# Optimization experiments

Hardware: AMD Instinct MI355X
Metric: run time of the kernel (lower is better)

The kernel has to match this reference:

```python
import jax, jax.numpy as jnp
import numpy as np

EPS = 1e-5  # torch LayerNorm default

def ln(x, g, b):
    mu = jnp.mean(x, axis=-1, keepdims=True)
    var = jnp.mean((x - mu) ** 2, axis=-1, keepdims=True)
    return (x - mu) * jax.lax.rsqrt(var + EPS) * g + b

B, S, E, A = 131072, 199, 3, 32
D_IN = S + 1  # state_dim + 1 (time feature)

def setup_inputs() -> dict:
    key = jax.random.key(0)
    ks = iter(jax.random.split(key, 32))
    def w(shape, fan_in):
        lim = 1.0 / np.sqrt(fan_in)
        return jax.random.uniform(next(ks), shape, jnp.float32, -lim, lim)
    inp = {
        "state": jax.random.normal(next(ks), (B, S), jnp.float32),
        "time_delta": jax.random.uniform(next(ks), (B,), jnp.float32),
        # trunk: Linear(200,256)+LN, Linear(256,256)+LN, Linear(256,128)+LN
        "W1": w((D_IN, 256), D_IN), "b1": w((256,), D_IN),
        "g1": jnp.ones((256,), jnp.float32), "be1": jnp.zeros((256,), jnp.float32),
        "W2": w((256, 256), 256), "b2": w((256,), 256),
        "g2": jnp.ones((256,), jnp.float32), "be2": jnp.zeros((256,), jnp.float32),
        "W3": w((256, 128), 256), "b3": w((128,), 256),
        "g3": jnp.ones((128,), jnp.float32), "be3": jnp.zeros((128,), jnp.float32),
        # value stream
        "Wv1": w((128, 64), 128), "bv1": w((64,), 128),
        "gv": jnp.ones((64,), jnp.float32), "bev": jnp.zeros((64,), jnp.float32),
        "Wv2": w((64, 1), 64), "bv2": w((1,), 64),
        # E stacked advantage streams (all heads share action dim A)
        "Wa1": w((E, 128, 64), 128), "ba1": w((E, 64), 128),
        "ga": jnp.ones((E, 64), jnp.float32), "bea": jnp.zeros((E, 64), jnp.float32),
        "Wa2": w((E, 64, A), 64), "ba2": w((E, A), 64),
        "event_type": jax.random.randint(next(ks), (B,), 0, E),
    }
    return inp

def reference(state, time_delta,
              W1, b1, g1, be1, W2, b2, g2, be2, W3, b3, g3, be3,
              Wv1, bv1, gv, bev, Wv2, bv2,
              Wa1, ba1, ga, bea, Wa2, ba2, event_type):
    td = time_delta[:, None]                       # [B,1]
    x = jnp.concatenate([state, td], axis=1)       # [B,200]
    h = jax.nn.relu(ln(x @ W1 + b1, g1, be1))      # [B,256]
    h = jax.nn.relu(ln(h @ W2 + b2, g2, be2))      # [B,256]
    f = jax.nn.relu(ln(h @ W3 + b3, g3, be3))      # [B,128]
    v = jax.nn.relu(ln(f @ Wv1 + bv1, gv, bev)) @ Wv2 + bv2  # [B,1]
    # compute all E advantage heads, then per-sample select by event_type
    h1 = jnp.einsum('bd,edh->ebh', f, Wa1) + ba1[:, None, :]           # [E,B,64]
    h1 = jax.nn.relu(ln(h1, ga[:, None, :], bea[:, None, :]))
    adv_all = jnp.einsum('ebh,eha->eba', h1, Wa2) + ba2[:, None, :]    # [E,B,A]
    adv = jnp.take_along_axis(adv_all, event_type[None, :, None], axis=0)[0]  # [B,A]
    return v + (adv - adv.mean(axis=1, keepdims=True))
```

## Files before the change

kernel.cpp:

```cpp
#include <hip/hip_runtime.h>
#include <hip/hip_bf16.h>
#include <stdint.h>

#define DEV __device__ __forceinline__

typedef __attribute__((ext_vector_type(8))) short short8;
typedef __attribute__((ext_vector_type(4))) float floatx4;

constexpr int TM  = 64;
constexpr int NB  = 131072;
constexpr int AST = 264;

struct F4 { float x,y,z,w; };

constexpr int OFF_W1 = 0;
constexpr int OFF_W2 = 57344;
constexpr int OFF_W3 = 122880;
constexpr int OFF_WH = 155648;
constexpr int OFF_WA2= 188416;
constexpr int NWQ    = 194560;

constexpr int C_B1=0, C_G1=256, C_BE1=512, C_B2=768, C_G2=1024, C_BE2=1280,
  C_B3=1536, C_G3=1664, C_BE3=1792, C_BV1=1920, C_GV=1984, C_BEV=2048,
  C_WV2=2112, C_BV2=2176, C_BA1=2180, C_GA=2372, C_BEA=2564, C_BA2=2756;
constexpr int NCONST=2852;

struct Ptrs {
  const float *state,*td,*W1,*b1,*g1,*be1,*W2,*b2,*g2,*be2,*W3,*b3,*g3,*be3,
    *Wv1,*bv1,*gv,*bev,*Wv2,*bv2,*Wa1,*ba1,*ga,*bea,*Wa2,*ba2;
  const int *et;
};

DEV unsigned short f2bf(float x){
  uint32_t u = __float_as_uint(x);
  u += 0x7fffu + ((u>>16)&1u);
  return (unsigned short)(u>>16);
}
DEV uint32_t pkbf(float a, float b){
  float2 f2; f2.x=a; f2.y=b;
  __hip_bfloat162 h = __float22bfloat162_rn(f2);
  union { __hip_bfloat162 h; uint32_t u; } cv; cv.h = h;
  return cv.u;
}

__global__ void prep_kernel(Ptrs p, unsigned short* __restrict__ wq, float* __restrict__ cq){
  int idx = blockIdx.x*256 + threadIdx.x;
  if (idx < NWQ) {
    float v = 0.f;
    if (idx < OFF_W2) {
      int e = idx, w = e/14336, r = e%14336;
      int kc = r>>11, ct=(r>>9)&3, l=(r>>3)&63, j=r&7;
      int n = w*64 + ct*16 + (l&15);
      int k = kc*32 + (l>>4)*8 + j;
      if (k < 200) v = p.W1[k*256 + n];
      else if (k == 200) v = p.b1[n];
    } else if (idx < OFF_W3) {
      int e = idx-OFF_W2, w=e>>14, r=e&16383;
      int kc=r>>11, ct=(r>>9)&3, l=(r>>3)&63, j=r&7;
      int n = w*64 + ct*16 + (l&15);
      int k = kc*32 + (l>>4)*8 + j;
      v = p.W2[k*256 + n];
    } else if (idx < OFF_WH) {
      int e = idx-OFF_W3, w=e>>13, r=e&8191;
      int kc=r>>10, ct=(r>>9)&1, l=(r>>3)&63, j=r&7;
      int n = w*32 + ct*16 + (l&15);
      int k = kc*32 + (l>>4)*8 + j;
      v = p.W3[k*128 + n];
    } else if (idx < OFF_WA2) {
      int e = idx-OFF_WH, h=e>>13, r=e&8191;
      int kc=r>>11, ct=(r>>9)&3, l=(r>>3)&63, j=r&7;
      int n = ct*16 + (l&15);
      int k = kc*32 + (l>>4)*8 + j;
      v = (h<3) ? p.Wa1[h*8192 + k*64 + n] : p.Wv1[k*64 + n];
    } else {
      int e = idx-OFF_WA2, h=e>>11, r=e&2047;
      int kc=r>>10, ct=(r>>9)&1, l=(r>>3)&63, j=r&7;
      int n = ct*16 + (l&15);
      int k = kc*32 + (l>>4)*8 + j;
      v = p.Wa2[h*2048 + k*32 + n];
    }
    wq[idx] = f2bf(v);
  } else if (idx < NWQ + NCONST) {
    int ci = idx - NWQ;
    float v;
    if      (ci < 256)  v = p.b1[ci];
    else if (ci < 512)  v = p.g1[ci-256];
    else if (ci < 768)  v = p.be1[ci-512];
    else if (ci < 1024) v = p.b2[ci-768];
    else if (ci < 1280) v = p.g2[ci-1024];
    else if (ci < 1536) v = p.be2[ci-1280];
    else if (ci < 1664) v = p.b3[ci-1536];
    else if (ci < 1792) v = p.g3[ci-1664];
    else if (ci < 1920) v = p.be3[ci-1792];
    else if (ci < 1984) v = p.bv1[ci-1920];
    else if (ci < 2048) v = p.gv[ci-1984];
    else if (ci < 2112) v = p.bev[ci-2048];
    else if (ci < 2176) v = p.Wv2[ci-2112];
    else if (ci < 2180) v = (ci==2176) ? p.bv2[0] : 0.f;
    else if (ci < 2372) v = p.ba1[ci-2180];
    else if (ci < 2564) v = p.ga[ci-2372];
    else if (ci < 2756) v = p.bea[ci-2564];
    else                v = p.ba2[ci-2756];
    cq[ci] = v;
  }
}

template<int RT>
DEV void zeroAccT(floatx4 (&acc)[RT][4]){
  const floatx4 z = {0.f,0.f,0.f,0.f};
  #pragma unroll
  for (int rt=0;rt<RT;rt++)
    #pragma unroll
    for (int ct=0;ct<4;ct++) acc[rt][ct]=z;
}

template<int KC,int RT>
DEV void runGemmW(floatx4 (&acc)[RT][4], const unsigned short* __restrict__ wp,
                  const unsigned short* __restrict__ aB, int aOff, int lane){
  #pragma unroll
  for (int kc=0;kc<KC;kc++){
    short8 a[4];
    #pragma unroll
    for (int c=0;c<4;c++)
      a[c] = *(const short8*)(aB + c*16*AST + aOff + kc*32);
    #pragma unroll
    for (int rt=0;rt<RT;rt++){
      short8 bw = *(const short8*)(wp + (kc*RT+rt)*512 + lane*8);
      #pragma unroll
      for (int c=0;c<4;c++)
        acc[rt][c] = __builtin_amdgcn_mfma_f32_16x16x32_bf16(bw, a[c], acc[rt][c], 0,0,0);
    }
  }
}

DEV void gemmL1G(floatx4 (&acc)[4][4], const unsigned short* __restrict__ wp,
                 const float* __restrict__ xb, const float* __restrict__ tdp,
                 int lane){
  const int q=lane>>4, ln=lane&15;
  #pragma unroll
  for (int kc=0;kc<7;kc++){
    short8 bfr[4];
    #pragma unroll
    for (int ct=0;ct<4;ct++){
      const float* rp = xb + (size_t)(ct*16+ln)*199;
      uint32_t w0,w1,w2,w3;
      if (kc<6){
        F4 lo = *(const F4*)(rp + kc*32 + q*8);
        F4 hi = *(const F4*)(rp + kc*32 + q*8 + 4);
        w0=pkbf(lo.x,lo.y); w1=pkbf(lo.z,lo.w); w2=pkbf(hi.x,hi.y); w3=pkbf(hi.z,hi.w);
      } else if (q==0){
        F4 lo = *(const F4*)(rp + 192);
        float v4=rp[196], v5=rp[197], v6=rp[198], v7=tdp[ct*16+ln];
        w0=pkbf(lo.x,lo.y); w1=pkbf(lo.z,lo.w); w2=pkbf(v4,v5); w3=pkbf(v6,v7);
      } else if (q==1){
        w0=0x3F80u; w1=0u; w2=0u; w3=0u;
      } else {
        w0=0u; w1=0u; w2=0u; w3=0u;
      }
      union { uint32_t u[4]; short8 s; } cv;
      cv.u[0]=w0; cv.u[1]=w1; cv.u[2]=w2; cv.u[3]=w3;
      bfr[ct]=cv.s;
    }
    #pragma unroll
    for (int rt=0;rt<4;rt++){
      short8 bw = *(const short8*)(wp + (kc*4+rt)*512 + lane*8);
      #pragma unroll
      for (int c=0;c<4;c++)
        acc[rt][c] = __builtin_amdgcn_mfma_f32_16x16x32_bf16(bw, bfr[c], acc[rt][c], 0,0,0);
    }
  }
}

template<int RT,bool BIAS>
DEV void statsT(floatx4 (&acc)[RT][4], const float* __restrict__ cq, int bo,
                float* sbuf, float* ssbuf, int q, int ln){
  if constexpr (BIAS){
    #pragma unroll
    for (int rt=0;rt<RT;rt++){
      floatx4 b4 = *(const floatx4*)(cq + bo + rt*16 + q*4);
      #pragma unroll
      for (int ct=0;ct<4;ct++) acc[rt][ct] += b4;
    }
  }
  #pragma unroll
  for (int ct=0;ct<4;ct++){
    float s=0.f, ss=0.f;
    #pragma unroll
    for (int rt=0;rt<RT;rt++)
      #pragma unroll
      for (int r=0;r<4;r++){ float v=acc[rt][ct][r]; s+=v; ss+=v*v; }
    s += __shfl_xor(s,16); ss += __shfl_xor(ss,16);
    s += __shfl_xor(s,32); ss += __shfl_xor(ss,32);
    if (q==0){
      atomicAdd(&sbuf[ct*16+ln], s);
      atomicAdd(&ssbuf[ct*16+ln], ss);
    }
  }
}

template<int RT>
DEV void lnWriteT(const floatx4 (&acc)[RT][4], const float* __restrict__ cq, int go, int beo,
                  const float* sbuf, const float* ssbuf, float invN,
                  unsigned short* act_, int colBase, int q, int ln){
  float mu[4], rs[4];
  #pragma unroll
  for (int ct=0;ct<4;ct++){
    float sv = sbuf[ct*16+ln], ssv = ssbuf[ct*16+ln];
    mu[ct] = sv*invN;
    rs[ct] = rsqrtf(ssv*invN - mu[ct]*mu[ct] + 1e-5f);
  }
  #pragma unroll
  for (int rt=0;rt<RT;rt++){
    floatx4 g4  = *(const floatx4*)(cq + go  + rt*16 + q*4);
    floatx4 be4 = *(const floatx4*)(cq + beo + rt*16 + q*4);
    #pragma unroll
    for (int ct=0;ct<4;ct++){
      float y[4];
      #pragma unroll
      for (int r=0;r<4;r++)
        y[r] = fmaxf((acc[rt][ct][r]-mu[ct])*rs[ct]*g4[r]+be4[r], 0.f);
      uint2 pk; pk.x = pkbf(y[0],y[1]); pk.y = pkbf(y[2],y[3]);
      *(uint2*)(act_ + (ct*16+ln)*AST + colBase + rt*16 + q*4) = pk;
    }
  }
}

DEV void headPhase(floatx4 (&acc)[4][4], const float* __restrict__ cq,
                   const unsigned short* __restrict__ wq,
                   const unsigned short* __restrict__ actb, float* vb,
                   int w, int lane, int q, int ln){
  zeroAccT<4>(acc);
  runGemmW<4,4>(acc, wq + OFF_WH + w*8192, actb + ln*AST + q*8, 0, lane);
  const int bo = (w<3)? C_BA1+w*64 : C_BV1;
  const int go = (w<3)? C_GA +w*64 : C_GV;
  const int beo= (w<3)? C_BEA+w*64 : C_BEV;
  #pragma unroll
  for (int rt=0;rt<4;rt++){
    floatx4 b4 = *(const floatx4*)(cq + bo + rt*16 + q*4);
    #pragma unroll
    for (int ct=0;ct<4;ct++) acc[rt][ct] += b4;
  }
  float mu[4], rs[4];
  #pragma unroll
  for (int ct=0;ct<4;ct++){
    float s=0.f, ss=0.f;
    #pragma unroll
    for (int rt=0;rt<4;rt++)
      #pragma unroll
      for (int r=0;r<4;r++){ float v=acc[rt][ct][r]; s+=v; ss+=v*v; }
    s += __shfl_xor(s,16); ss += __shfl_xor(ss,16);
    s += __shfl_xor(s,32); ss += __shfl_xor(ss,32);
    mu[ct]=s*(1.f/64.f);
    rs[ct]=rsqrtf(ss*(1.f/64.f)-mu[ct]*mu[ct]+1e-5f);
  }
  #pragma unroll
  for (int rt=0;rt<4;rt++){
    floatx4 g4  = *(const floatx4*)(cq + go  + rt*16 + q*4);
    floatx4 be4 = *(const floatx4*)(cq + beo + rt*16 + q*4);
    #pragma unroll
    for (int ct=0;ct<4;ct++)
      #pragma unroll
      for (int r=0;r<4;r++)
        acc[rt][ct][r] = fmaxf((acc[rt][ct][r]-mu[ct])*rs[ct]*g4[r]+be4[r], 0.f);
  }
  if (w==3){
    float bv2v = cq[C_BV2];
    floatx4 wv4[4];
    #pragma unroll
    for (int rt=0;rt<4;rt++) wv4[rt] = *(const floatx4*)(cq + C_WV2 + rt*16 + q*4);
    #pragma unroll
    for (int ct=0;ct<4;ct++){
      float dot=0.f;
      #pragma unroll
      for (int rt=0;rt<4;rt++)
        #pragma unroll
        for (int r=0;r<4;r++) dot += acc[rt][ct][r]*wv4[rt][r];
      dot += __shfl_xor(dot,16);
      dot += __shfl_xor(dot,32);
      if (q==0) vb[ct*16+ln] = dot + bv2v;
    }
  }
}

DEV void advPhase(const floatx4 (&acc)[4][4], const float* __restrict__ cq,
                  const unsigned short* __restrict__ wq,
                  unsigned short* actb, const float* vb, const int* etlT,
                  float* __restrict__ outT, int w, int lane, int q, int ln){
  #pragma unroll
  for (int rt=0;rt<4;rt++)
    #pragma unroll
    for (int ct=0;ct<4;ct++){
      uint2 pk;
      pk.x = pkbf(acc[rt][ct][0], acc[rt][ct][1]);
      pk.y = pkbf(acc[rt][ct][2], acc[rt][ct][3]);
      *(uint2*)(actb + (ct*16+ln)*AST + 64*w + rt*16 + q*4) = pk;
    }
  floatx4 acc2[2][4];
  zeroAccT<2>(acc2);
  runGemmW<2,2>(acc2, wq + OFF_WA2 + w*2048, actb + ln*AST + q*8, 64*w, lane);
  #pragma unroll
  for (int rt=0;rt<2;rt++){
    floatx4 b4 = *(const floatx4*)(cq + C_BA2 + w*32 + rt*16 + q*4);
    #pragma unroll
    for (int ct=0;ct<4;ct++) acc2[rt][ct] += b4;
  }
  #pragma unroll
  for (int ct=0;ct<4;ct++){
    float sm=0.f;
    #pragma unroll
    for (int rt=0;rt<2;rt++)
      #pragma unroll
      for (int r=0;r<4;r++) sm += acc2[rt][ct][r];
    sm += __shfl_xor(sm,16);
    sm += __shfl_xor(sm,32);
    int b = ct*16+ln;
    if (etlT[b]==w){
      float vm = vb[b] - sm*(1.f/32.f);
      #pragma unroll
      for (int rt=0;rt<2;rt++){
        floatx4 o = acc2[rt][ct];
        o[0]+=vm; o[1]+=vm; o[2]+=vm; o[3]+=vm;
        *(floatx4*)(outT + (size_t)b*32 + rt*16 + q*4) = o;
      }
    }
  }
}

__global__ __launch_bounds__(256,2) void dqn_main(
    const float* __restrict__ state, const float* __restrict__ td,
    const int* __restrict__ et, const unsigned short* __restrict__ wq,
    const float* __restrict__ cq, float* __restrict__ out)
{
  __shared__ __align__(16) unsigned short actA[TM*AST];
  __shared__ __align__(16) unsigned short actB[TM*AST];
  __shared__ float sstat[2][3][2][64];
  __shared__ float vbuf[2][64];
  __shared__ int   etl[2][64];

  const int tid=threadIdx.x, w=tid>>6, lane=tid&63, q=lane>>4, ln=lane&15;
  const int rowBlk = blockIdx.x*128;
  const float* x0 = state + (size_t)rowBlk*199;
  const float* x1 = x0 + (size_t)64*199;

  ((float*)sstat)[tid]     = 0.f;
  ((float*)sstat)[tid+256] = 0.f;
  ((float*)sstat)[tid+512] = 0.f;
  if (tid < 128) ((int*)etl)[tid] = et[rowBlk+tid];
  __syncthreads();

  floatx4 aT0[4][4], aT1[4][4];

  zeroAccT<4>(aT0);
  gemmL1G(aT0, wq + OFF_W1 + w*14336, x0, td + rowBlk, lane);
  statsT<4,false>(aT0, cq, 0, sstat[0][0][0], sstat[0][0][1], q, ln);
  __syncthreads();

  lnWriteT<4>(aT0, cq, C_G1+w*64, C_BE1+w*64, sstat[0][0][0], sstat[0][0][1], 1.f/256.f, actA, w*64, q, ln);
  zeroAccT<4>(aT1);
  gemmL1G(aT1, wq + OFF_W1 + w*14336, x1, td + rowBlk + 64, lane);
  statsT<4,false>(aT1, cq, 0, sstat[1][0][0], sstat[1][0][1], q, ln);
  __syncthreads();

  lnWriteT<4>(aT1, cq, C_G1+w*64, C_BE1+w*64, sstat[1][0][0], sstat[1][0][1], 1.f/256.f, actB, w*64, q, ln);
  zeroAccT<4>(aT0);
  runGemmW<8,4>(aT0, wq + OFF_W2 + w*16384, actA + ln*AST + q*8, 0, lane);
  statsT<4,true>(aT0, cq, C_B2+w*64, sstat[0][1][0], sstat[0][1][1], q, ln);
  __syncthreads();

  lnWriteT<4>(aT0, cq, C_G2+w*64, C_BE2+w*64, sstat[0][1][0], sstat[0][1][1], 1.f/256.f, actA, w*64, q, ln);
  zeroAccT<4>(aT1);
  runGemmW<8,4>(aT1, wq + OFF_W2 + w*16384, actB + ln*AST + q*8, 0, lane);
  statsT<4,true>(aT1, cq, C_B2+w*64, sstat[1][1][0], sstat[1][1][1], q, ln);
  __syncthreads();

  lnWriteT<4>(aT1, cq, C_G2+w*64, C_BE2+w*64, sstat[1][1][0], sstat[1][1][1], 1.f/256.f, actB, w*64, q, ln);
  floatx4 c3T0[2][4];
  zeroAccT<2>(c3T0);
  runGemmW<8,2>(c3T0, wq + OFF_W3 + w*8192, actA + ln*AST + q*8, 0, lane);
  statsT<2,true>(c3T0, cq, C_B3+w*32, sstat[0][2][0], sstat[0][2][1], q, ln);
  __syncthreads();

  lnWriteT<2>(c3T0, cq, C_G3+w*32, C_BE3+w*32, sstat[0][2][0], sstat[0][2][1], 1.f/128.f, actA, w*32, q, ln);
  floatx4 c3T1[2][4];
  zeroAccT<2>(c3T1);
  runGemmW<8,2>(c3T1, wq + OFF_W3 + w*8192, actB + ln*AST + q*8, 0, lane);
  statsT<2,true>(c3T1, cq, C_B3+w*32, sstat[1][2][0], sstat[1][2][1], q, ln);
  __syncthreads();

  lnWriteT<2>(c3T1, cq, C_G3+w*32, C_BE3+w*32, sstat[1][2][0], sstat[1][2][1], 1.f/128.f, actB, w*32, q, ln);
  headPhase(aT0, cq, wq, actA, vbuf[0], w, lane, q, ln);
  __syncthreads();

  headPhase(aT1, cq, wq, actB, vbuf[1], w, lane, q, ln);
  if (w<3) advPhase(aT0, cq, wq, actA, vbuf[0], etl[0], out + (size_t)rowBlk*32, w, lane, q, ln);
  __syncthreads();

  if (w<3) advPhase(aT1, cq, wq, actB, vbuf[1], etl[1], out + (size_t)(rowBlk+64)*32, w, lane, q, ln);
}

extern "C" void kernel_launch(void* const* d_in, const int* in_sizes, int n_in,
                              void* d_out, int out_size, void* d_ws, size_t ws_size,
                              hipStream_t stream)
{
  Ptrs p;
  p.state=(const float*)d_in[0];  p.td =(const float*)d_in[1];
  p.W1 =(const float*)d_in[2];  p.b1 =(const float*)d_in[3];  p.g1 =(const float*)d_in[4];  p.be1=(const float*)d_in[5];
  p.W2 =(const float*)d_in[6];  p.b2 =(const float*)d_in[7];  p.g2 =(const float*)d_in[8];  p.be2=(const float*)d_in[9];
  p.W3 =(const float*)d_in[10]; p.b3 =(const float*)d_in[11]; p.g3 =(const float*)d_in[12]; p.be3=(const float*)d_in[13];
  p.Wv1=(const float*)d_in[14]; p.bv1=(const float*)d_in[15]; p.gv =(const float*)d_in[16]; p.bev=(const float*)d_in[17];
  p.Wv2=(const float*)d_in[18]; p.bv2=(const float*)d_in[19];
  p.Wa1=(const float*)d_in[20]; p.ba1=(const float*)d_in[21]; p.ga =(const float*)d_in[22]; p.bea=(const float*)d_in[23];
  p.Wa2=(const float*)d_in[24]; p.ba2=(const float*)d_in[25];
  p.et =(const int*)d_in[26];

  unsigned short* wq = (unsigned short*)d_ws;
  float* cq = (float*)((char*)d_ws + (size_t)NWQ*2);

  const int prepN = NWQ + NCONST;
  hipLaunchKernelGGL(prep_kernel, dim3((prepN+255)/256), dim3(256), 0, stream, p, wq, cq);
  hipLaunchKernelGGL(dqn_main, dim3(NB/128), dim3(256), 0, stream,
                     p.state, p.td, p.et, (const unsigned short*)wq, (const float*)cq, (float*)d_out);
}
```

Measured before the change: 291.5 us.

## Process one 64-row tile per block with register weight prefetch and higher occupancy

```diff
diff --git a/kernel.cpp b/kernel.cpp
--- a/kernel.cpp
+++ b/kernel.cpp
@@ -115,6 +115,41 @@
 }
 
 template<int KC,int RT>
+DEV void runGemmPF(floatx4 (&acc)[RT][4], const unsigned short* __restrict__ wp,
+                   const unsigned short* __restrict__ aB, int aOff, int lane,
+                   const short8 (&pf)[4]){
+  constexpr int PFK = 4/RT;
+  constexpr int NBLK = KC/PFK;
+  short8 wcur[4];
+  #pragma unroll
+  for (int i=0;i<4;i++) wcur[i]=pf[i];
+  #pragma unroll
+  for (int blk=0; blk<NBLK; blk++){
+    short8 wnxt[4];
+    if (blk+1 < NBLK){
+      #pragma unroll
+      for (int i=0;i<4;i++)
+        wnxt[i] = *(const short8*)(wp + ((blk+1)*4 + i)*512 + lane*8);
+    }
+    #pragma unroll
+    for (int kk=0;kk<PFK;kk++){
+      const int kc = blk*PFK+kk;
+      short8 a[4];
+      #pragma unroll
+      for (int c=0;c<4;c++)
+        a[c] = *(const short8*)(aB + c*16*AST + aOff + kc*32);
+      #pragma unroll
+      for (int rt=0;rt<RT;rt++)
+        #pragma unroll
+        for (int c=0;c<4;c++)
+          acc[rt][c] = __builtin_amdgcn_mfma_f32_16x16x32_bf16(wcur[kk*RT+rt], a[c], acc[rt][c], 0,0,0);
+    }
+    #pragma unroll
+    for (int i=0;i<4;i++) wcur[i]=wnxt[i];
+  }
+}
+
+template<int KC,int RT>
 DEV void runGemmW(floatx4 (&acc)[RT][4], const unsigned short* __restrict__ wp,
                   const unsigned short* __restrict__ aB, int aOff, int lane){
   #pragma unroll
@@ -133,12 +168,21 @@
   }
 }
 
-DEV void gemmL1G(floatx4 (&acc)[4][4], const unsigned short* __restrict__ wp,
-                 const float* __restrict__ xb, const float* __restrict__ tdp,
-                 int lane){
+DEV void gemmL1Gpf(floatx4 (&acc)[4][4], const unsigned short* __restrict__ wp,
+                   const float* __restrict__ xb, const float* __restrict__ tdp,
+                   int lane, const short8 (&pf)[4]){
   const int q=lane>>4, ln=lane&15;
+  short8 wcur[4];
+  #pragma unroll
+  for (int i=0;i<4;i++) wcur[i]=pf[i];
   #pragma unroll
   for (int kc=0;kc<7;kc++){
+    short8 wnxt[4];
+    if (kc<6){
+      #pragma unroll
+      for (int rt=0;rt<4;rt++)
+        wnxt[rt] = *(const short8*)(wp + ((kc+1)*4+rt)*512 + lane*8);
+    }
     short8 bfr[4];
     #pragma unroll
     for (int ct=0;ct<4;ct++){
@@ -162,18 +206,18 @@
       bfr[ct]=cv.s;
     }
     #pragma unroll
-    for (int rt=0;rt<4;rt++){
-      short8 bw = *(const short8*)(wp + (kc*4+rt)*512 + lane*8);
+    for (int rt=0;rt<4;rt++)
       #pragma unroll
       for (int c=0;c<4;c++)
-        acc[rt][c] = __builtin_amdgcn_mfma_f32_16x16x32_bf16(bw, bfr[c], acc[rt][c], 0,0,0);
-    }
+        acc[rt][c] = __builtin_amdgcn_mfma_f32_16x16x32_bf16(wcur[rt], bfr[c], acc[rt][c], 0,0,0);
+    #pragma unroll
+    for (int i=0;i<4;i++) wcur[i]=wnxt[i];
   }
 }
 
 template<int RT,bool BIAS>
-DEV void statsT(floatx4 (&acc)[RT][4], const float* __restrict__ cq, int bo,
-                float* sbuf, float* ssbuf, int q, int ln){
+DEV void statsS(floatx4 (&acc)[RT][4], const float* __restrict__ cq, int bo,
+                float (*sst)[64][4], int w, int q, int ln){
   if constexpr (BIAS){
     #pragma unroll
     for (int rt=0;rt<RT;rt++){
@@ -192,22 +236,26 @@
     s += __shfl_xor(s,16); ss += __shfl_xor(ss,16);
     s += __shfl_xor(s,32); ss += __shfl_xor(ss,32);
     if (q==0){
-      atomicAdd(&sbuf[ct*16+ln], s);
-      atomicAdd(&ssbuf[ct*16+ln], ss);
+      sst[0][ct*16+ln][w] = s;
+      sst[1][ct*16+ln][w] = ss;
     }
   }
 }
 
 template<int RT>
-DEV void lnWriteT(const floatx4 (&acc)[RT][4], const float* __restrict__ cq, int go, int beo,
-                  const float* sbuf, const float* ssbuf, float invN,
+DEV void lnWriteS(const floatx4 (&acc)[RT][4], const float* __restrict__ cq, int go, int beo,
+                  const float (*sst)[64][4], float invN,
                   unsigned short* act_, int colBase, int q, int ln){
   float mu[4], rs[4];
   #pragma unroll
   for (int ct=0;ct<4;ct++){
-    float sv = sbuf[ct*16+ln], ssv = ssbuf[ct*16+ln];
+    int row = ct*16+ln;
+    floatx4 s4 = *(const floatx4*)&sst[0][row][0];
+    floatx4 q4 = *(const floatx4*)&sst[1][row][0];
+    float sv = s4[0]+s4[1]+s4[2]+s4[3];
+    float qv = q4[0]+q4[1]+q4[2]+q4[3];
     mu[ct] = sv*invN;
-    rs[ct] = rsqrtf(ssv*invN - mu[ct]*mu[ct] + 1e-5f);
+    rs[ct] = rsqrtf(qv*invN - mu[ct]*mu[ct] + 1e-5f);
   }
   #pragma unroll
   for (int rt=0;rt<RT;rt++){
@@ -225,177 +273,159 @@
   }
 }
 
-DEV void headPhase(floatx4 (&acc)[4][4], const float* __restrict__ cq,
-                   const unsigned short* __restrict__ wq,
-                   const unsigned short* __restrict__ actb, float* vb,
-                   int w, int lane, int q, int ln){
-  zeroAccT<4>(acc);
-  runGemmW<4,4>(acc, wq + OFF_WH + w*8192, actb + ln*AST + q*8, 0, lane);
-  const int bo = (w<3)? C_BA1+w*64 : C_BV1;
-  const int go = (w<3)? C_GA +w*64 : C_GV;
-  const int beo= (w<3)? C_BEA+w*64 : C_BEV;
-  #pragma unroll
-  for (int rt=0;rt<4;rt++){
-    floatx4 b4 = *(const floatx4*)(cq + bo + rt*16 + q*4);
-    #pragma unroll
-    for (int ct=0;ct<4;ct++) acc[rt][ct] += b4;
-  }
-  float mu[4], rs[4];
-  #pragma unroll
-  for (int ct=0;ct<4;ct++){
-    float s=0.f, ss=0.f;
-    #pragma unroll
-    for (int rt=0;rt<4;rt++)
-      #pragma unroll
-      for (int r=0;r<4;r++){ float v=acc[rt][ct][r]; s+=v; ss+=v*v; }
-    s += __shfl_xor(s,16); ss += __shfl_xor(ss,16);
-    s += __shfl_xor(s,32); ss += __shfl_xor(ss,32);
-    mu[ct]=s*(1.f/64.f);
-    rs[ct]=rsqrtf(ss*(1.f/64.f)-mu[ct]*mu[ct]+1e-5f);
-  }
-  #pragma unroll
-  for (int rt=0;rt<4;rt++){
-    floatx4 g4  = *(const floatx4*)(cq + go  + rt*16 + q*4);
-    floatx4 be4 = *(const floatx4*)(cq + beo + rt*16 + q*4);
-    #pragma unroll
-    for (int ct=0;ct<4;ct++)
-      #pragma unroll
-      for (int r=0;r<4;r++)
-        acc[rt][ct][r] = fmaxf((acc[rt][ct][r]-mu[ct])*rs[ct]*g4[r]+be4[r], 0.f);
-  }
-  if (w==3){
-    float bv2v = cq[C_BV2];
-    floatx4 wv4[4];
-    #pragma unroll
-    for (int rt=0;rt<4;rt++) wv4[rt] = *(const floatx4*)(cq + C_WV2 + rt*16 + q*4);
-    #pragma unroll
-    for (int ct=0;ct<4;ct++){
-      float dot=0.f;
-      #pragma unroll
-      for (int rt=0;rt<4;rt++)
-        #pragma unroll
-        for (int r=0;r<4;r++) dot += acc[rt][ct][r]*wv4[rt][r];
-      dot += __shfl_xor(dot,16);
-      dot += __shfl_xor(dot,32);
-      if (q==0) vb[ct*16+ln] = dot + bv2v;
-    }
-  }
-}
-
-DEV void advPhase(const floatx4 (&acc)[4][4], const float* __restrict__ cq,
-                  const unsigned short* __restrict__ wq,
-                  unsigned short* actb, const float* vb, const int* etlT,
-                  float* __restrict__ outT, int w, int lane, int q, int ln){
-  #pragma unroll
-  for (int rt=0;rt<4;rt++)
-    #pragma unroll
-    for (int ct=0;ct<4;ct++){
-      uint2 pk;
-      pk.x = pkbf(acc[rt][ct][0], acc[rt][ct][1]);
-      pk.y = pkbf(acc[rt][ct][2], acc[rt][ct][3]);
-      *(uint2*)(actb + (ct*16+ln)*AST + 64*w + rt*16 + q*4) = pk;
-    }
-  floatx4 acc2[2][4];
-  zeroAccT<2>(acc2);
-  runGemmW<2,2>(acc2, wq + OFF_WA2 + w*2048, actb + ln*AST + q*8, 64*w, lane);
-  #pragma unroll
-  for (int rt=0;rt<2;rt++){
-    floatx4 b4 = *(const floatx4*)(cq + C_BA2 + w*32 + rt*16 + q*4);
-    #pragma unroll
-    for (int ct=0;ct<4;ct++) acc2[rt][ct] += b4;
-  }
-  #pragma unroll
-  for (int ct=0;ct<4;ct++){
-    float sm=0.f;
-    #pragma unroll
-    for (int rt=0;rt<2;rt++)
-      #pragma unroll
-      for (int r=0;r<4;r++) sm += acc2[rt][ct][r];
-    sm += __shfl_xor(sm,16);
-    sm += __shfl_xor(sm,32);
-    int b = ct*16+ln;
-    if (etlT[b]==w){
-      float vm = vb[b] - sm*(1.f/32.f);
-      #pragma unroll
-      for (int rt=0;rt<2;rt++){
-        floatx4 o = acc2[rt][ct];
-        o[0]+=vm; o[1]+=vm; o[2]+=vm; o[3]+=vm;
-        *(floatx4*)(outT + (size_t)b*32 + rt*16 + q*4) = o;
-      }
-    }
-  }
-}
-
-__global__ __launch_bounds__(256,2) void dqn_main(
+__global__ __launch_bounds__(256,4) void dqn_main(
     const float* __restrict__ state, const float* __restrict__ td,
     const int* __restrict__ et, const unsigned short* __restrict__ wq,
     const float* __restrict__ cq, float* __restrict__ out)
 {
-  __shared__ __align__(16) unsigned short actA[TM*AST];
-  __shared__ __align__(16) unsigned short actB[TM*AST];
-  __shared__ float sstat[2][3][2][64];
-  __shared__ float vbuf[2][64];
-  __shared__ int   etl[2][64];
+  __shared__ __align__(16) unsigned short act[TM*AST];
+  __shared__ __align__(16) float sstat[2][64][4];
+  __shared__ float vbuf[64];
 
   const int tid=threadIdx.x, w=tid>>6, lane=tid&63, q=lane>>4, ln=lane&15;
-  const int rowBlk = blockIdx.x*128;
+  const int rowBlk = blockIdx.x*TM;
   const float* x0 = state + (size_t)rowBlk*199;
-  const float* x1 = x0 + (size_t)64*199;
-
-  ((float*)sstat)[tid]     = 0.f;
-  ((float*)sstat)[tid+256] = 0.f;
-  ((float*)sstat)[tid+512] = 0.f;
-  if (tid < 128) ((int*)etl)[tid] = et[rowBlk+tid];
-  __syncthreads();
-
-  floatx4 aT0[4][4], aT1[4][4];
-
-  zeroAccT<4>(aT0);
-  gemmL1G(aT0, wq + OFF_W1 + w*14336, x0, td + rowBlk, lane);
-  statsT<4,false>(aT0, cq, 0, sstat[0][0][0], sstat[0][0][1], q, ln);
-  __syncthreads();
-
-  lnWriteT<4>(aT0, cq, C_G1+w*64, C_BE1+w*64, sstat[0][0][0], sstat[0][0][1], 1.f/256.f, actA, w*64, q, ln);
-  zeroAccT<4>(aT1);
-  gemmL1G(aT1, wq + OFF_W1 + w*14336, x1, td + rowBlk + 64, lane);
-  statsT<4,false>(aT1, cq, 0, sstat[1][0][0], sstat[1][0][1], q, ln);
-  __syncthreads();
-
-  lnWriteT<4>(aT1, cq, C_G1+w*64, C_BE1+w*64, sstat[1][0][0], sstat[1][0][1], 1.f/256.f, actB, w*64, q, ln);
-  zeroAccT<4>(aT0);
-  runGemmW<8,4>(aT0, wq + OFF_W2 + w*16384, actA + ln*AST + q*8, 0, lane);
-  statsT<4,true>(aT0, cq, C_B2+w*64, sstat[0][1][0], sstat[0][1][1], q, ln);
-  __syncthreads();
-
-  lnWriteT<4>(aT0, cq, C_G2+w*64, C_BE2+w*64, sstat[0][1][0], sstat[0][1][1], 1.f/256.f, actA, w*64, q, ln);
-  zeroAccT<4>(aT1);
-  runGemmW<8,4>(aT1, wq + OFF_W2 + w*16384, actB + ln*AST + q*8, 0, lane);
-  statsT<4,true>(aT1, cq, C_B2+w*64, sstat[1][1][0], sstat[1][1][1], q, ln);
-  __syncthreads();
-
-  lnWriteT<4>(aT1, cq, C_G2+w*64, C_BE2+w*64, sstat[1][1][0], sstat[1][1][1], 1.f/256.f, actB, w*64, q, ln);
-  floatx4 c3T0[2][4];
-  zeroAccT<2>(c3T0);
-  runGemmW<8,2>(c3T0, wq + OFF_W3 + w*8192, actA + ln*AST + q*8, 0, lane);
-  statsT<2,true>(c3T0, cq, C_B3+w*32, sstat[0][2][0], sstat[0][2][1], q, ln);
-  __syncthreads();
-
-  lnWriteT<2>(c3T0, cq, C_G3+w*32, C_BE3+w*32, sstat[0][2][0], sstat[0][2][1], 1.f/128.f, actA, w*32, q, ln);
-  floatx4 c3T1[2][4];
-  zeroAccT<2>(c3T1);
-  runGemmW<8,2>(c3T1, wq + OFF_W3 + w*8192, actB + ln*AST + q*8, 0, lane);
-  statsT<2,true>(c3T1, cq, C_B3+w*32, sstat[1][2][0], sstat[1][2][1], q, ln);
-  __syncthreads();
-
-  lnWriteT<2>(c3T1, cq, C_G3+w*32, C_BE3+w*32, sstat[1][2][0], sstat[1][2][1], 1.f/128.f, actB, w*32, q, ln);
-  headPhase(aT0, cq, wq, actA, vbuf[0], w, lane, q, ln);
-  __syncthreads();
-
-  headPhase(aT1, cq, wq, actB, vbuf[1], w, lane, q, ln);
-  if (w<3) advPhase(aT0, cq, wq, actA, vbuf[0], etl[0], out + (size_t)rowBlk*32, w, lane, q, ln);
-  __syncthreads();
-
-  if (w<3) advPhase(aT1, cq, wq, actB, vbuf[1], etl[1], out + (size_t)(rowBlk+64)*32, w, lane, q, ln);
+
+  const unsigned short* wl1 = wq + OFF_W1 + w*14336;
+  const unsigned short* wl2 = wq + OFF_W2 + w*16384;
+  const unsigned short* wl3 = wq + OFF_W3 + w*8192;
+  const unsigned short* wlh = wq + OFF_WH + w*8192;
+  const unsigned short* aBase = act + ln*AST + q*8;
+
+  short8 pf[4];
+  floatx4 acc[4][4];
+
+  #pragma unroll
+  for (int i=0;i<4;i++) pf[i] = *(const short8*)(wl1 + i*512 + lane*8);
+  zeroAccT<4>(acc);
+  gemmL1Gpf(acc, wl1, x0, td + rowBlk, lane, pf);
+  statsS<4,false>(acc, cq, 0, sstat, w, q, ln);
+  __syncthreads();
+
+  #pragma unroll
+  for (int i=0;i<4;i++) pf[i] = *(const short8*)(wl2 + i*512 + lane*8);
+  lnWriteS<4>(acc, cq, C_G1+w*64, C_BE1+w*64, sstat, 1.f/256.f, act, w*64, q, ln);
+  __syncthreads();
+
+  zeroAccT<4>(acc);
+  runGemmPF<8,4>(acc, wl2, aBase, 0, lane, pf);
+  statsS<4,true>(acc, cq, C_B2+w*64, sstat, w, q, ln);
+  __syncthreads();
+
+  #pragma unroll
+  for (int i=0;i<4;i++) pf[i] = *(const short8*)(wl3 + i*512 + lane*8);
+  lnWriteS<4>(acc, cq, C_G2+w*64, C_BE2+w*64, sstat, 1.f/256.f, act, w*64, q, ln);
+  __syncthreads();
+
+  floatx4 acc3[2][4];
+  zeroAccT<2>(acc3);
+  runGemmPF<8,2>(acc3, wl3, aBase, 0, lane, pf);
+  statsS<2,true>(acc3, cq, C_B3+w*32, sstat, w, q, ln);
+  __syncthreads();
+
+  #pragma unroll
+  for (int i=0;i<4;i++) pf[i] = *(const short8*)(wlh + i*512 + lane*8);
+  lnWriteS<2>(acc3, cq, C_G3+w*32, C_BE3+w*32, sstat, 1.f/128.f, act, w*32, q, ln);
+  __syncthreads();
+
+  zeroAccT<4>(acc);
+  runGemmPF<4,4>(acc, wlh, aBase, 0, lane, pf);
+  {
+    const int bo = (w<3)? C_BA1+w*64 : C_BV1;
+    const int go = (w<3)? C_GA +w*64 : C_GV;
+    const int beo= (w<3)? C_BEA+w*64 : C_BEV;
+    #pragma unroll
+    for (int rt=0;rt<4;rt++){
+      floatx4 b4 = *(const floatx4*)(cq + bo + rt*16 + q*4);
+      #pragma unroll
+      for (int ct=0;ct<4;ct++) acc[rt][ct] += b4;
+    }
+    float mu[4], rs[4];
+    #pragma unroll
+    for (int ct=0;ct<4;ct++){
+      float s=0.f, ss=0.f;
+      #pragma unroll
+      for (int rt=0;rt<4;rt++)
+        #pragma unroll
+        for (int r=0;r<4;r++){ float v=acc[rt][ct][r]; s+=v; ss+=v*v; }
+      s += __shfl_xor(s,16); ss += __shfl_xor(ss,16);
+      s += __shfl_xor(s,32); ss += __shfl_xor(ss,32);
+      mu[ct]=s*(1.f/64.f);
+      rs[ct]=rsqrtf(ss*(1.f/64.f)-mu[ct]*mu[ct]+1e-5f);
+    }
+    #pragma unroll
+    for (int rt=0;rt<4;rt++){
+      floatx4 g4  = *(const floatx4*)(cq + go  + rt*16 + q*4);
+      floatx4 be4 = *(const floatx4*)(cq + beo + rt*16 + q*4);
+      #pragma unroll
+      for (int ct=0;ct<4;ct++)
+        #pragma unroll
+        for (int r=0;r<4;r++)
+          acc[rt][ct][r] = fmaxf((acc[rt][ct][r]-mu[ct])*rs[ct]*g4[r]+be4[r], 0.f);
+    }
+    if (w==3){
+      float bv2v = cq[C_BV2];
+      floatx4 wv4[4];
+      #pragma unroll
+      for (int rt=0;rt<4;rt++) wv4[rt] = *(const floatx4*)(cq + C_WV2 + rt*16 + q*4);
+      #pragma unroll
+      for (int ct=0;ct<4;ct++){
+        float dot=0.f;
+        #pragma unroll
+        for (int rt=0;rt<4;rt++)
+          #pragma unroll
+          for (int r=0;r<4;r++) dot += acc[rt][ct][r]*wv4[rt][r];
+        dot += __shfl_xor(dot,16);
+        dot += __shfl_xor(dot,32);
+        if (q==0) vbuf[ct*16+ln] = dot + bv2v;
+      }
+    }
+  }
+  __syncthreads();
+
+  if (w<3){
+    #pragma unroll
+    for (int rt=0;rt<4;rt++)
+      #pragma unroll
+      for (int ct=0;ct<4;ct++){
+        uint2 pk;
+        pk.x = pkbf(acc[rt][ct][0], acc[rt][ct][1]);
+        pk.y = pkbf(acc[rt][ct][2], acc[rt][ct][3]);
+        *(uint2*)(act + (ct*16+ln)*AST + 64*w + rt*16 + q*4) = pk;
+      }
+    int ev[4];
+    #pragma unroll
+    for (int ct=0;ct<4;ct++) ev[ct] = et[rowBlk + ct*16 + ln];
+    floatx4 acc2[2][4];
+    zeroAccT<2>(acc2);
+    runGemmW<2,2>(acc2, wq + OFF_WA2 + w*2048, aBase, 64*w, lane);
+    #pragma unroll
+    for (int rt=0;rt<2;rt++){
+      floatx4 b4 = *(const floatx4*)(cq + C_BA2 + w*32 + rt*16 + q*4);
+      #pragma unroll
+      for (int ct=0;ct<4;ct++) acc2[rt][ct] += b4;
+    }
+    #pragma unroll
+    for (int ct=0;ct<4;ct++){
+      float sm=0.f;
+      #pragma unroll
+      for (int rt=0;rt<2;rt++)
+        #pragma unroll
+        for (int r=0;r<4;r++) sm += acc2[rt][ct][r];
+      sm += __shfl_xor(sm,16);
+      sm += __shfl_xor(sm,32);
+      int b = ct*16+ln;
+      if (ev[ct]==w){
+        float vm = vbuf[b] - sm*(1.f/32.f);
+        #pragma unroll
+        for (int rt=0;rt<2;rt++){
+          floatx4 o = acc2[rt][ct];
+          o[0]+=vm; o[1]+=vm; o[2]+=vm; o[3]+=vm;
+          *(floatx4*)(out + (size_t)(rowBlk+b)*32 + rt*16 + q*4) = o;
+        }
+      }
+    }
+  }
 }
 
 extern "C" void kernel_launch(void* const* d_in, const int* in_sizes, int n_in,
@@ -418,6 +448,6 @@
 
   const int prepN = NWQ + NCONST;
   hipLaunchKernelGGL(prep_kernel, dim3((prepN+255)/256), dim3(256), 0, stream, p, wq, cq);
-  hipLaunchKernelGGL(dqn_main, dim3(NB/128), dim3(256), 0, stream,
+  hipLaunchKernelGGL(dqn_main, dim3(NB/TM), dim3(256), 0, stream,
                      p.state, p.td, p.et, (const unsigned short*)wq, (const float*)cq, (float*)d_out);
 }
```

Measured after the change: 299.2 us. +2.7%, slower.
